# Kernel optimization log

Measured on AMD Instinct MI355X. Metric: run time of the kernel, lower is better.

The kernel has to match this reference:

```python
import jax, jax.numpy as jnp
import numpy as np

IN_FEATURES = 4096
OUT_FEATURES = 4096


def setup_inputs() -> dict:
    key = jax.random.key(0)
    kx, kw = jax.random.split(key)
    x = jax.random.normal(kx, (4, 2048, IN_FEATURES), dtype=jnp.float32)
    # matches nn.Parameter(torch.randn(out, in) * 0.01)
    weight = jax.random.normal(kw, (OUT_FEATURES, IN_FEATURES), dtype=jnp.float32) * 0.01
    return {"x": x, "weight": weight}


def reference(x, weight):
    # STE: forward uses sign(weight); gradient passes straight through to weight.
    w_q = jnp.sign(weight)
    weight_proxy = weight + jax.lax.stop_gradient(w_q - weight)
    # F.linear(x, W) = x @ W.T ; [b, s, in] x [out, in] -> [b, s, out]
    return jnp.einsum('bsi,oi->bso', x, weight_proxy)
```

## Files before the change

### kernel.cpp

```cpp
#include <hip/hip_runtime.h>
#include <hip/hip_bf16.h>


#define M_DIM 8192
#define N_DIM 4096
#define K_DIM 4096
#define BM 256
#define BN 256
#define BK 64
#define NT (K_DIM / BK)
#define TILES_M (M_DIM / BM)
#define TILES_N (N_DIM / BN)

typedef __bf16 bf16x8 __attribute__((ext_vector_type(8)));
typedef float f32x4 __attribute__((ext_vector_type(4)));

__device__ __forceinline__ void gload_lds16(const __bf16* g, __bf16* l) {
    __builtin_amdgcn_global_load_lds(
        (const __attribute__((address_space(1))) void*)g,
        (__attribute__((address_space(3))) void*)l, 16, 0, 0);
}


__global__ __launch_bounds__(256) void quant_x_k(const float* __restrict__ x,
                                                 __bf16* __restrict__ xq, int n8) {
    int stride = gridDim.x * blockDim.x;
    for (int i = blockIdx.x * blockDim.x + threadIdx.x; i < n8; i += stride) {
        float4 v0 = reinterpret_cast<const float4*>(x)[2 * (size_t)i];
        float4 v1 = reinterpret_cast<const float4*>(x)[2 * (size_t)i + 1];
        bf16x8 o;
        o[0] = (__bf16)v0.x; o[1] = (__bf16)v0.y; o[2] = (__bf16)v0.z; o[3] = (__bf16)v0.w;
        o[4] = (__bf16)v1.x; o[5] = (__bf16)v1.y; o[6] = (__bf16)v1.z; o[7] = (__bf16)v1.w;
        *reinterpret_cast<bf16x8*>(xq + 8 * (size_t)i) = o;
    }
}

__global__ __launch_bounds__(256) void quant_w_k(const float* __restrict__ w,
                                                 __bf16* __restrict__ wq, int n8) {
    int stride = gridDim.x * blockDim.x;
    for (int i = blockIdx.x * blockDim.x + threadIdx.x; i < n8; i += stride) {
        float4 v0 = reinterpret_cast<const float4*>(w)[2 * (size_t)i];
        float4 v1 = reinterpret_cast<const float4*>(w)[2 * (size_t)i + 1];
        float f[8] = {v0.x, v0.y, v0.z, v0.w, v1.x, v1.y, v1.z, v1.w};
        bf16x8 o;
#pragma unroll
        for (int j = 0; j < 8; ++j)
            o[j] = (__bf16)((f[j] > 0.f) ? 1.f : ((f[j] < 0.f) ? -1.f : 0.f));
        *reinterpret_cast<bf16x8*>(wq + 8 * (size_t)i) = o;
    }
}


__global__ __launch_bounds__(512, 2) void gemm256_k(const __bf16* __restrict__ A,
                                                    const __bf16* __restrict__ B,
                                                    float* __restrict__ C) {
    extern __shared__ __bf16 sm[];
    __bf16* As = sm;
    __bf16* Bs = sm + 32768;

    int bid = blockIdx.x;
    int cpx = (TILES_M * TILES_N) >> 3;
    int swz = (bid & 7) * cpx + (bid >> 3);
    int bm = swz / TILES_N, bn = swz % TILES_N;
    const __bf16* Ag = A + (size_t)bm * BM * K_DIM;
    const __bf16* Bg = B + (size_t)bn * BN * K_DIM;

    int tid = threadIdx.x;
    int wave = tid >> 6, lane = tid & 63;
    int wm = wave >> 2, wn = wave & 3;
    int lr = lane & 15, lq = lane >> 4;
    int laneRow = lane >> 3;
    int gslot8 = (((lane & 7) ^ laneRow) << 3);
    int swc0 = ((0 * 4 + lq) ^ (lr & 7)) << 3;
    int swc1 = ((1 * 4 + lq) ^ (lr & 7)) << 3;

    f32x4 acc[8][4];
#pragma unroll
    for (int m = 0; m < 8; ++m)
#pragma unroll
        for (int n = 0; n < 4; ++n) acc[m][n] = (f32x4)(0.f);

#define STAGE(gbase, ldsbase, kt_) do {                                               \
        const __bf16* g0_ = (gbase) + (size_t)(wave * 8 + laneRow) * K_DIM            \
                            + ((kt_) * BK + gslot8);                                  \
        gload_lds16(g0_, (ldsbase) + wave * 512);                                     \
        gload_lds16(g0_ + (size_t)64 * K_DIM, (ldsbase) + (wave + 8) * 512);          \
    } while (0)

    STAGE(Bg, Bs + 0 * 8192, 0);
    STAGE(Bg + (size_t)128 * K_DIM, Bs + 1 * 8192, 0);
    STAGE(Ag, As + 0 * 8192, 0);
    STAGE(Ag + (size_t)128 * K_DIM, As + 1 * 8192, 0);
    STAGE(Bg, Bs + 2 * 8192, 1);
    STAGE(Bg + (size_t)128 * K_DIM, Bs + 3 * 8192, 1);
    asm volatile("s_waitcnt vmcnt(4)" ::: "memory");
    __builtin_amdgcn_s_barrier();

    for (int kt = 0; kt < NT; ++kt) {
        int b = kt & 1;
        int ktn = (kt + 1) & (NT - 1);
        int ktnn = (kt + 2) & (NT - 1);
        const __bf16* ap = As + (b * 2 + wm) * 8192;
        const __bf16* bp = Bs + (b * 2 + (wn >> 1)) * 8192;
        int brow_ = (wn & 1) * 64;

        bf16x8 bfr[4][2];
#pragma unroll
        for (int q = 0; q < 4; ++q) {
            bf16x8 afr[2][2];
#pragma unroll
            for (int m2 = 0; m2 < 2; ++m2) {
                const __bf16* r = ap + ((2 * q + m2) * 16 + lr) * 64;
                afr[m2][0] = *reinterpret_cast<const bf16x8*>(r + swc0);
                afr[m2][1] = *reinterpret_cast<const bf16x8*>(r + swc1);
            }
            if (q == 0) {
#pragma unroll
                for (int n = 0; n < 4; ++n) {
                    const __bf16* r = bp + (brow_ + n * 16 + lr) * 64;
                    bfr[n][0] = *reinterpret_cast<const bf16x8*>(r + swc0);
                    bfr[n][1] = *reinterpret_cast<const bf16x8*>(r + swc1);
                }
            }
            if (q == 0)      STAGE(Ag,                         As + ((b ^ 1) * 2 + 0) * 8192, ktn);
            else if (q == 1) STAGE(Ag + (size_t)128 * K_DIM,   As + ((b ^ 1) * 2 + 1) * 8192, ktn);
            else if (q == 2) STAGE(Bg,                         Bs + (b * 2 + 0) * 8192, ktnn);
            else             STAGE(Bg + (size_t)128 * K_DIM,   Bs + (b * 2 + 1) * 8192, ktnn);

            __builtin_amdgcn_s_barrier();
            asm volatile("s_waitcnt lgkmcnt(0)" ::: "memory");
            __builtin_amdgcn_s_setprio(1);
#pragma unroll
            for (int m2 = 0; m2 < 2; ++m2)
#pragma unroll
                for (int n = 0; n < 4; ++n)
#pragma unroll
                    for (int ks = 0; ks < 2; ++ks)
                        acc[2 * q + m2][n] = __builtin_amdgcn_mfma_f32_16x16x32_bf16(
                            afr[m2][ks], bfr[n][ks], acc[2 * q + m2][n], 0, 0, 0);
            __builtin_amdgcn_s_setprio(0);
            if (q == 3) asm volatile("s_waitcnt vmcnt(4)" ::: "memory");
            __builtin_amdgcn_s_barrier();
        }
    }
#undef STAGE

    size_t crow0 = (size_t)bm * BM + wm * 128 + lq * 4;
    size_t ccol0 = (size_t)bn * BN + wn * 64 + lr;
#pragma unroll
    for (int m = 0; m < 8; ++m)
#pragma unroll
        for (int n = 0; n < 4; ++n) {
            float* cp = C + (crow0 + m * 16) * N_DIM + (ccol0 + n * 16);
#pragma unroll
            for (int j = 0; j < 4; ++j) cp[(size_t)j * N_DIM] = acc[m][n][j];
        }
}

extern "C" void kernel_launch(void* const* d_in, const int* in_sizes, int n_in,
                              void* d_out, int out_size, void* d_ws, size_t ws_size,
                              hipStream_t stream) {
    const float* x = (const float*)d_in[0];
    const float* w = (const float*)d_in[1];
    float* out = (float*)d_out;

    __bf16* xq = (__bf16*)d_ws;
    __bf16* wq = xq + (size_t)M_DIM * K_DIM;

    hipFuncSetAttribute((const void*)gemm256_k,
                        hipFuncAttributeMaxDynamicSharedMemorySize, 131072);

    quant_x_k<<<2048, 256, 0, stream>>>(x, xq, (M_DIM * K_DIM) / 8);
    quant_w_k<<<1024, 256, 0, stream>>>(w, wq, (N_DIM * K_DIM) / 8);
    gemm256_k<<<TILES_M * TILES_N, 512, 131072, stream>>>(xq, wq, out);
}
```

Baseline: 476.6 us.

## Switch GEMM to 32x32x16 MFMA with A-fragment prefetch and LDS-staged epilogue

Replaces the 16x16x32 bf16 MFMA tiling with 32x32x16 MFMAs, giving each wave 4x2 32x32 accumulator tiles. A fragments are double-buffered in registers (aP/aQ) so the LDS reads for the next sub-tile overlap the current MFMA phase, with partial lgkmcnt waits and sched_barriers. The epilogue now transposes each accumulator tile through LDS scratch so global stores are 16-byte row-contiguous instead of strided scalar writes. The larger MFMA shape cuts LDS read traffic per FLOP, but the changed register pressure and the extra barriers could hurt occupancy or scheduling.

```diff
diff --git a/kernel.cpp b/kernel.cpp
--- a/kernel.cpp
+++ b/kernel.cpp
@@ -14,6 +14,7 @@
 
 typedef __bf16 bf16x8 __attribute__((ext_vector_type(8)));
 typedef float f32x4 __attribute__((ext_vector_type(4)));
+typedef float f32x16 __attribute__((ext_vector_type(16)));
 
 __device__ __forceinline__ void gload_lds16(const __bf16* g, __bf16* l) {
     __builtin_amdgcn_global_load_lds(
@@ -68,23 +69,63 @@
     int tid = threadIdx.x;
     int wave = tid >> 6, lane = tid & 63;
     int wm = wave >> 2, wn = wave & 3;
-    int lr = lane & 15, lq = lane >> 4;
+    int l31 = lane & 31, l7 = lane & 7, hi = lane >> 5;
     int laneRow = lane >> 3;
-    int gslot8 = (((lane & 7) ^ laneRow) << 3);
-    int swc0 = ((0 * 4 + lq) ^ (lr & 7)) << 3;
-    int swc1 = ((1 * 4 + lq) ^ (lr & 7)) << 3;
-
-    f32x4 acc[8][4];
-#pragma unroll
-    for (int m = 0; m < 8; ++m)
-#pragma unroll
-        for (int n = 0; n < 4; ++n) acc[m][n] = (f32x4)(0.f);
+    int gslot8 = ((l7 ^ laneRow) << 3);
+    int bro = (wn & 1) * 64;
+
+    int swk0 = (((0 + hi) ^ l7) << 3);
+    int swk1 = (((2 + hi) ^ l7) << 3);
+    int swk2 = (((4 + hi) ^ l7) << 3);
+    int swk3 = (((6 + hi) ^ l7) << 3);
+
+    f32x16 acc[4][2];
+#pragma unroll
+    for (int m = 0; m < 4; ++m)
+#pragma unroll
+        for (int n = 0; n < 2; ++n) acc[m][n] = (f32x16)(0.f);
+
+    bf16x8 bfr[2][4];
+    bf16x8 aP[4], aQ[4];
 
 #define STAGE(gbase, ldsbase, kt_) do {                                               \
         const __bf16* g0_ = (gbase) + (size_t)(wave * 8 + laneRow) * K_DIM            \
                             + ((kt_) * BK + gslot8);                                  \
         gload_lds16(g0_, (ldsbase) + wave * 512);                                     \
         gload_lds16(g0_ + (size_t)64 * K_DIM, (ldsbase) + (wave + 8) * 512);          \
+    } while (0)
+
+#define RD_A(dst, base_, mt_) do {                                                    \
+        const __bf16* r_ = (base_) + ((mt_) * 32 + l31) * 64;                         \
+        dst[0] = *reinterpret_cast<const bf16x8*>(r_ + swk0);                         \
+        dst[1] = *reinterpret_cast<const bf16x8*>(r_ + swk1);                         \
+        dst[2] = *reinterpret_cast<const bf16x8*>(r_ + swk2);                         \
+        dst[3] = *reinterpret_cast<const bf16x8*>(r_ + swk3);                         \
+    } while (0)
+
+#define RD_B(base_) do {                                                              \
+        const __bf16* r0_ = (base_) + (bro + l31) * 64;                               \
+        const __bf16* r1_ = (base_) + (bro + 32 + l31) * 64;                          \
+        bfr[0][0] = *reinterpret_cast<const bf16x8*>(r0_ + swk0);                     \
+        bfr[0][1] = *reinterpret_cast<const bf16x8*>(r0_ + swk1);                     \
+        bfr[0][2] = *reinterpret_cast<const bf16x8*>(r0_ + swk2);                     \
+        bfr[0][3] = *reinterpret_cast<const bf16x8*>(r0_ + swk3);                     \
+        bfr[1][0] = *reinterpret_cast<const bf16x8*>(r1_ + swk0);                     \
+        bfr[1][1] = *reinterpret_cast<const bf16x8*>(r1_ + swk1);                     \
+        bfr[1][2] = *reinterpret_cast<const bf16x8*>(r1_ + swk2);                     \
+        bfr[1][3] = *reinterpret_cast<const bf16x8*>(r1_ + swk3);                     \
+    } while (0)
+
+#define MFMA_PHASE(MT, AR) do {                                                       \
+        __builtin_amdgcn_s_setprio(1);                                                \
+        _Pragma("unroll")                                                             \
+        for (int ks = 0; ks < 4; ++ks) {                                              \
+            acc[MT][0] = __builtin_amdgcn_mfma_f32_32x32x16_bf16(                     \
+                AR[ks], bfr[0][ks], acc[MT][0], 0, 0, 0);                             \
+            acc[MT][1] = __builtin_amdgcn_mfma_f32_32x32x16_bf16(                     \
+                AR[ks], bfr[1][ks], acc[MT][1], 0, 0, 0);                             \
+        }                                                                             \
+        __builtin_amdgcn_s_setprio(0);                                                \
     } while (0)
 
     STAGE(Bg, Bs + 0 * 8192, 0);
@@ -96,64 +137,85 @@
     asm volatile("s_waitcnt vmcnt(4)" ::: "memory");
     __builtin_amdgcn_s_barrier();
 
+    {
+        const __bf16* ap0 = As + wm * 8192;
+        const __bf16* bp0 = Bs + (wn >> 1) * 8192;
+        RD_B(bp0);
+        RD_A(aP, ap0, 0);
+    }
+
     for (int kt = 0; kt < NT; ++kt) {
         int b = kt & 1;
         int ktn = (kt + 1) & (NT - 1);
         int ktnn = (kt + 2) & (NT - 1);
         const __bf16* ap = As + (b * 2 + wm) * 8192;
         const __bf16* bp = Bs + (b * 2 + (wn >> 1)) * 8192;
-        int brow_ = (wn & 1) * 64;
-
-        bf16x8 bfr[4][2];
-#pragma unroll
-        for (int q = 0; q < 4; ++q) {
-            bf16x8 afr[2][2];
-#pragma unroll
-            for (int m2 = 0; m2 < 2; ++m2) {
-                const __bf16* r = ap + ((2 * q + m2) * 16 + lr) * 64;
-                afr[m2][0] = *reinterpret_cast<const bf16x8*>(r + swc0);
-                afr[m2][1] = *reinterpret_cast<const bf16x8*>(r + swc1);
+
+        RD_A(aQ, ap, 1);
+        STAGE(Ag, As + ((b ^ 1) * 2 + 0) * 8192, ktn);
+        __builtin_amdgcn_s_barrier();
+        asm volatile("s_waitcnt lgkmcnt(4)" ::: "memory");
+        __builtin_amdgcn_sched_barrier(0);
+        MFMA_PHASE(0, aP);
+        __builtin_amdgcn_s_barrier();
+
+        RD_A(aP, ap, 2);
+        STAGE(Ag + (size_t)128 * K_DIM, As + ((b ^ 1) * 2 + 1) * 8192, ktn);
+        __builtin_amdgcn_s_barrier();
+        asm volatile("s_waitcnt lgkmcnt(4)" ::: "memory");
+        __builtin_amdgcn_sched_barrier(0);
+        MFMA_PHASE(1, aQ);
+        __builtin_amdgcn_s_barrier();
+
+        RD_A(aQ, ap, 3);
+        STAGE(Bg, Bs + (b * 2 + 0) * 8192, ktnn);
+        __builtin_amdgcn_s_barrier();
+        asm volatile("s_waitcnt lgkmcnt(4)" ::: "memory");
+        __builtin_amdgcn_sched_barrier(0);
+        MFMA_PHASE(2, aP);
+        __builtin_amdgcn_s_barrier();
+
+        STAGE(Bg + (size_t)128 * K_DIM, Bs + (b * 2 + 1) * 8192, ktnn);
+        __builtin_amdgcn_s_barrier();
+        asm volatile("s_waitcnt lgkmcnt(0)" ::: "memory");
+        __builtin_amdgcn_sched_barrier(0);
+        MFMA_PHASE(3, aQ);
+        asm volatile("s_waitcnt vmcnt(4)" ::: "memory");
+        __builtin_amdgcn_s_barrier();
+        if (kt + 1 < NT) {
+            const __bf16* apn = As + ((b ^ 1) * 2 + wm) * 8192;
+            const __bf16* bpn = Bs + ((b ^ 1) * 2 + (wn >> 1)) * 8192;
+            RD_B(bpn);
+            RD_A(aP, apn, 0);
+        }
+    }
+#undef STAGE
+#undef RD_A
+#undef RD_B
+#undef MFMA_PHASE
+
+    asm volatile("s_waitcnt vmcnt(0)" ::: "memory");
+    __builtin_amdgcn_s_barrier();
+
+    float* scr = reinterpret_cast<float*>(sm) + wave * 1024;
+    size_t crow0 = (size_t)bm * BM + wm * 128;
+    size_t ccol0 = (size_t)bn * BN + wn * 64;
+#pragma unroll
+    for (int mt = 0; mt < 4; ++mt)
+#pragma unroll
+        for (int nt = 0; nt < 2; ++nt) {
+#pragma unroll
+            for (int j = 0; j < 16; ++j) {
+                int r = (j & 3) + 8 * (j >> 2) + 4 * hi;
+                scr[r * 32 + l31] = acc[mt][nt][j];
             }
-            if (q == 0) {
-#pragma unroll
-                for (int n = 0; n < 4; ++n) {
-                    const __bf16* r = bp + (brow_ + n * 16 + lr) * 64;
-                    bfr[n][0] = *reinterpret_cast<const bf16x8*>(r + swc0);
-                    bfr[n][1] = *reinterpret_cast<const bf16x8*>(r + swc1);
-                }
+#pragma unroll
+            for (int p = 0; p < 4; ++p) {
+                int r = p * 8 + (lane >> 3);
+                f32x4 v = *reinterpret_cast<const f32x4*>(scr + r * 32 + l7 * 4);
+                *reinterpret_cast<f32x4*>(C + (crow0 + mt * 32 + r) * N_DIM
+                                          + ccol0 + nt * 32 + l7 * 4) = v;
             }
-            if (q == 0)      STAGE(Ag,                         As + ((b ^ 1) * 2 + 0) * 8192, ktn);
-            else if (q == 1) STAGE(Ag + (size_t)128 * K_DIM,   As + ((b ^ 1) * 2 + 1) * 8192, ktn);
-            else if (q == 2) STAGE(Bg,                         Bs + (b * 2 + 0) * 8192, ktnn);
-            else             STAGE(Bg + (size_t)128 * K_DIM,   Bs + (b * 2 + 1) * 8192, ktnn);
-
-            __builtin_amdgcn_s_barrier();
-            asm volatile("s_waitcnt lgkmcnt(0)" ::: "memory");
-            __builtin_amdgcn_s_setprio(1);
-#pragma unroll
-            for (int m2 = 0; m2 < 2; ++m2)
-#pragma unroll
-                for (int n = 0; n < 4; ++n)
-#pragma unroll
-                    for (int ks = 0; ks < 2; ++ks)
-                        acc[2 * q + m2][n] = __builtin_amdgcn_mfma_f32_16x16x32_bf16(
-                            afr[m2][ks], bfr[n][ks], acc[2 * q + m2][n], 0, 0, 0);
-            __builtin_amdgcn_s_setprio(0);
-            if (q == 3) asm volatile("s_waitcnt vmcnt(4)" ::: "memory");
-            __builtin_amdgcn_s_barrier();
-        }
-    }
-#undef STAGE
-
-    size_t crow0 = (size_t)bm * BM + wm * 128 + lq * 4;
-    size_t ccol0 = (size_t)bn * BN + wn * 64 + lr;
-#pragma unroll
-    for (int m = 0; m < 8; ++m)
-#pragma unroll
-        for (int n = 0; n < 4; ++n) {
-            float* cp = C + (crow0 + m * 16) * N_DIM + (ccol0 + n * 16);
-#pragma unroll
-            for (int j = 0; j < 4; ++j) cp[(size_t)j * N_DIM] = acc[m][n][j];
         }
 }
 
```

Result: slower. 519.0 us (+8.9%).
